# Kernel tuning notes

Measured on AMD Instinct MI355X. Metric: run time of the kernel, lower is better.

Reference implementation:

```python
import jax, jax.numpy as jnp
import numpy as np

N_NODES = 100000
N_EDGES = 500000
D = 128


def setup_inputs() -> dict:
    key = jax.random.key(0)
    ks = jax.random.split(key, 6)
    x = jax.random.normal(ks[0], (N_NODES, D), dtype=jnp.float32)
    edge_index = jax.random.randint(ks[1], (2, N_EDGES), 0, N_NODES, dtype=jnp.int64)
    edge_label = jax.random.randint(ks[2], (N_EDGES,), 0, 2, dtype=jnp.int64)
    # MLP params (dim_in -> dim_in, 2 layers, has_act=True, has_bias=True)
    scale = 1.0 / np.sqrt(D)
    W1 = jax.random.normal(ks[3], (D, D), dtype=jnp.float32) * scale
    b1 = jnp.zeros((D,), dtype=jnp.float32)
    W2 = jax.random.normal(ks[4], (D, D), dtype=jnp.float32) * scale
    b2 = jnp.zeros((D,), dtype=jnp.float32)
    return {"x": x, "edge_index": edge_index, "edge_label": edge_label,
            "W1": W1, "b1": b1, "W2": W2, "b2": b2}


def reference(x, edge_index, edge_label, W1, b1, W2, b2):
    # post-MP MLP on all node features (has_act=True -> ReLU after each layer)
    h = jax.nn.relu(x @ W1 + b1)          # [N, D]
    h = jax.nn.relu(h @ W2 + b2)          # [N, D]
    # gather endpoints: batch.x[edge_index] -> [2, E, D]
    v1 = h[edge_index[0]]                  # [E, D]
    v2 = h[edge_index[1]]                  # [E, D]
    # dot decode: sum(v1 * v2, dim=-1)
    pred = jnp.sum(v1 * v2, axis=-1)       # [E]
    return pred, edge_label
```

## Files before the change

### kernel.cpp

```cpp
#include <hip/hip_runtime.h>

typedef __attribute__((ext_vector_type(8))) short short8;
typedef __attribute__((ext_vector_type(4))) float floatx4;

#define D 128
#define NWAVES 4

__device__ unsigned short g_wq[2 * D * D];

__device__ __forceinline__ unsigned short f2bf(float f) {
  unsigned u = __float_as_uint(f);
  u += 0x7FFFu + ((u >> 16) & 1u);
  return (unsigned short)(u >> 16);
}

__global__ __launch_bounds__(256) void prep_w(const float* __restrict__ W1,
                                              const float* __restrict__ W2) {
  const int t = blockIdx.x * 256 + threadIdx.x;
  const int layer = t >> 14;
  const int r = t & 16383;
  const int fragid = r >> 9;
  const int lane = (r >> 3) & 63;
  const int e = r & 7;
  const int kk = fragid >> 3, n0 = fragid & 7;
  const int k = kk * 32 + (lane >> 4) * 8 + e;
  const int n = n0 * 16 + (lane & 15);
  const float* W = layer ? W2 : W1;
  g_wq[t] = f2bf(W[k * D + n]);
}

__device__ __forceinline__ short8 cvt_a(const floatx4& f0, const floatx4& f1) {
  short8 a;
  a[0] = (short)f2bf(f0[0]); a[1] = (short)f2bf(f0[1]);
  a[2] = (short)f2bf(f0[2]); a[3] = (short)f2bf(f0[3]);
  a[4] = (short)f2bf(f1[0]); a[5] = (short)f2bf(f1[1]);
  a[6] = (short)f2bf(f1[2]); a[7] = (short)f2bf(f1[3]);
  return a;
}

__global__ __launch_bounds__(256, 2) void mlp_fused(
    const float* __restrict__ x,
    const float* __restrict__ b1, const float* __restrict__ b2,
    unsigned short* __restrict__ h, int nNodes, int npairs) {
  __shared__ unsigned short sH[NWAVES][16 * D];
  const int tid = threadIdx.x;
  const int wave = tid >> 6, lane = tid & 63;
  const int quad = lane >> 4, l16 = lane & 15;

  const int p = blockIdx.x * NWAVES + wave;
  if (p >= npairs) return;

  const short8* wq1 = (const short8*)g_wq;
  const short8* wq2 = (const short8*)(g_wq + 16384);
  unsigned short* mysH = sH[wave];

  const int mbase = p * 32;
  const int m0 = mbase + l16;
  const int m1 = m0 + 16;
  short8 a0[4], a1[4];
  {
    const floatx4* xp0 = (const floatx4*)(x + (size_t)m0 * D + quad * 8);
    const floatx4* xp1 = (const floatx4*)(x + (size_t)m1 * D + quad * 8);
    const bool v0 = (m0 < nNodes), v1 = (m1 < nNodes);
    floatx4 xf0[8], xf1[8];
    #pragma unroll
    for (int i = 0; i < 8; ++i) {
      const int o = (i >> 1) * 8 + (i & 1);
      xf0[i] = v0 ? xp0[o] : (floatx4){0.f, 0.f, 0.f, 0.f};
      xf1[i] = v1 ? xp1[o] : (floatx4){0.f, 0.f, 0.f, 0.f};
    }
    #pragma unroll
    for (int kk = 0; kk < 4; ++kk) {
      a0[kk] = cvt_a(xf0[2 * kk], xf0[2 * kk + 1]);
      a1[kk] = cvt_a(xf1[2 * kk], xf1[2 * kk + 1]);
    }
  }
  short8 bf[32];
  #pragma unroll
  for (int i = 0; i < 32; ++i) bf[i] = wq1[i * 64 + lane];
  __builtin_amdgcn_sched_barrier(0);
  floatx4 acc0[8], acc1[8];
  #pragma unroll
  for (int n0 = 0; n0 < 8; ++n0) {
    acc0[n0] = (floatx4){0.f, 0.f, 0.f, 0.f};
    acc1[n0] = (floatx4){0.f, 0.f, 0.f, 0.f};
  }
  #pragma unroll
  for (int kk = 0; kk < 4; ++kk) {
    #pragma unroll
    for (int n0 = 0; n0 < 8; ++n0) {
      acc0[n0] = __builtin_amdgcn_mfma_f32_16x16x32_bf16(a0[kk], bf[kk * 8 + n0], acc0[n0], 0, 0, 0);
      acc1[n0] = __builtin_amdgcn_mfma_f32_16x16x32_bf16(a1[kk], bf[kk * 8 + n0], acc1[n0], 0, 0, 0);
    }
  }
  __builtin_amdgcn_sched_barrier(0);
  #pragma unroll
  for (int i = 0; i < 32; ++i) bf[i] = wq2[i * 64 + lane];
  __builtin_amdgcn_sched_barrier(0);
  float bias1[8];
  #pragma unroll
  for (int n0 = 0; n0 < 8; ++n0) bias1[n0] = b1[n0 * 16 + l16];
  short8 af0[4], af1[4];
  #pragma unroll
  for (int n0 = 0; n0 < 8; ++n0) {
    #pragma unroll
    for (int r = 0; r < 4; ++r) {
      float v = acc0[n0][r] + bias1[n0];
      v = v > 0.f ? v : 0.f;
      const int row = quad * 4 + r;
      const int g = 2 * n0 + (l16 >> 3);
      mysH[row * D + (((g ^ row) & 15) << 3) + (l16 & 7)] = f2bf(v);
    }
  }
  #pragma unroll
  for (int kk = 0; kk < 4; ++kk)
    af0[kk] = *(const short8*)&mysH[l16 * D + ((((kk * 4 + quad) ^ l16) & 15) << 3)];
  #pragma unroll
  for (int n0 = 0; n0 < 8; ++n0) {
    #pragma unroll
    for (int r = 0; r < 4; ++r) {
      float v = acc1[n0][r] + bias1[n0];
      v = v > 0.f ? v : 0.f;
      const int row = quad * 4 + r;
      const int g = 2 * n0 + (l16 >> 3);
      mysH[row * D + (((g ^ row) & 15) << 3) + (l16 & 7)] = f2bf(v);
    }
  }
  #pragma unroll
  for (int kk = 0; kk < 4; ++kk)
    af1[kk] = *(const short8*)&mysH[l16 * D + ((((kk * 4 + quad) ^ l16) & 15) << 3)];
  #pragma unroll
  for (int n0 = 0; n0 < 8; ++n0) {
    acc0[n0] = (floatx4){0.f, 0.f, 0.f, 0.f};
    acc1[n0] = (floatx4){0.f, 0.f, 0.f, 0.f};
  }
  #pragma unroll
  for (int kk = 0; kk < 4; ++kk) {
    #pragma unroll
    for (int n0 = 0; n0 < 8; ++n0) {
      acc0[n0] = __builtin_amdgcn_mfma_f32_16x16x32_bf16(af0[kk], bf[kk * 8 + n0], acc0[n0], 0, 0, 0);
      acc1[n0] = __builtin_amdgcn_mfma_f32_16x16x32_bf16(af1[kk], bf[kk * 8 + n0], acc1[n0], 0, 0, 0);
    }
  }
  __builtin_amdgcn_sched_barrier(0);
  float bias2[8];
  #pragma unroll
  for (int n0 = 0; n0 < 8; ++n0) bias2[n0] = b2[n0 * 16 + l16];
  #pragma unroll
  for (int n0 = 0; n0 < 8; ++n0) {
    #pragma unroll
    for (int r = 0; r < 4; ++r) {
      float v = acc0[n0][r] + bias2[n0];
      v = v > 0.f ? v : 0.f;
      const int row = quad * 4 + r;
      const int g = 2 * n0 + (l16 >> 3);
      mysH[row * D + (((g ^ row) & 15) << 3) + (l16 & 7)] = f2bf(v);
    }
  }
  #pragma unroll
  for (int i = 0; i < 4; ++i) {
    const int row = i * 4 + quad;
    short8 vrow = *(const short8*)&mysH[row * D + (((l16 ^ row) & 15) << 3)];
    const int g = mbase + row;
    if (g < nNodes) *(short8*)&h[(size_t)g * D + l16 * 8] = vrow;
  }
  #pragma unroll
  for (int n0 = 0; n0 < 8; ++n0) {
    #pragma unroll
    for (int r = 0; r < 4; ++r) {
      float v = acc1[n0][r] + bias2[n0];
      v = v > 0.f ? v : 0.f;
      const int row = quad * 4 + r;
      const int g = 2 * n0 + (l16 >> 3);
      mysH[row * D + (((g ^ row) & 15) << 3) + (l16 & 7)] = f2bf(v);
    }
  }
  #pragma unroll
  for (int i = 0; i < 4; ++i) {
    const int row = i * 4 + quad;
    short8 vrow = *(const short8*)&mysH[row * D + (((l16 ^ row) & 15) << 3)];
    const int g = mbase + 16 + row;
    if (g < nNodes) *(short8*)&h[(size_t)g * D + l16 * 8] = vrow;
  }
}

__device__ __forceinline__ float dot2bf(unsigned a, unsigned b, float acc) {
  float a0 = __uint_as_float(a << 16);
  float a1 = __uint_as_float(a & 0xFFFF0000u);
  float b0 = __uint_as_float(b << 16);
  float b1 = __uint_as_float(b & 0xFFFF0000u);
  acc = fmaf(a0, b0, acc);
  acc = fmaf(a1, b1, acc);
  return acc;
}

__device__ __forceinline__ float edge_dot(const uint4& a, const uint4& b) {
  float acc = 0.f;
  acc = dot2bf(a.x, b.x, acc);
  acc = dot2bf(a.y, b.y, acc);
  acc = dot2bf(a.z, b.z, acc);
  acc = dot2bf(a.w, b.w, acc);
  acc += __shfl_xor(acc, 8);
  acc += __shfl_xor(acc, 4);
  acc += __shfl_xor(acc, 2);
  acc += __shfl_xor(acc, 1);
  return acc;
}

__global__ __launch_bounds__(256) void edge_kernel(
    const unsigned short* __restrict__ h2, const int* __restrict__ eidx,
    const int* __restrict__ elabel, float* __restrict__ out, int E) {
  const int t = blockIdx.x * 256 + threadIdx.x;
  {
    const int E4 = E & ~3;
    for (int li = t * 4; li < E4; li += gridDim.x * 256 * 4) {
      int4 lv = *(const int4*)&elabel[li];
      float4 fv = make_float4((float)lv.x, (float)lv.y, (float)lv.z, (float)lv.w);
      *(float4*)&out[E + li] = fv;
    }
    if (t < (E & 3)) out[E + E4 + t] = (float)elabel[E4 + t];
  }
  const int sub = threadIdx.x & 15;
  const int grp = t >> 4;
  const int e0 = grp * 8;
  if (e0 + 8 <= E) {
    const int4 s0 = *(const int4*)&eidx[e0];
    const int4 s1 = *(const int4*)&eidx[e0 + 4];
    const int4 t0 = *(const int4*)&eidx[E + e0];
    const int4 t1 = *(const int4*)&eidx[E + e0 + 4];
    int s[8] = {s0.x, s0.y, s0.z, s0.w, s1.x, s1.y, s1.z, s1.w};
    int d[8] = {t0.x, t0.y, t0.z, t0.w, t1.x, t1.y, t1.z, t1.w};
    uint4 va[8], vb[8];
    #pragma unroll
    for (int i = 0; i < 8; ++i) {
      va[i] = *(const uint4*)(h2 + (((size_t)(unsigned)s[i]) << 7) + sub * 8);
      vb[i] = *(const uint4*)(h2 + (((size_t)(unsigned)d[i]) << 7) + sub * 8);
    }
    #pragma unroll
    for (int i = 0; i < 8; ++i) {
      float acc = edge_dot(va[i], vb[i]);
      if (sub == 0) out[e0 + i] = acc;
    }
  } else if (e0 < E) {
    for (int e = e0; e < E; ++e) {
      const int s = eidx[e];
      const int d = eidx[E + e];
      const uint4 ua = *(const uint4*)(h2 + (((size_t)(unsigned)s) << 7) + sub * 8);
      const uint4 ub = *(const uint4*)(h2 + (((size_t)(unsigned)d) << 7) + sub * 8);
      float acc = edge_dot(ua, ub);
      if (sub == 0) out[e] = acc;
    }
  }
}

extern "C" void kernel_launch(void* const* d_in, const int* in_sizes, int n_in,
                              void* d_out, int out_size, void* d_ws, size_t ws_size,
                              hipStream_t stream) {
  const float* x  = (const float*)d_in[0];
  const int* eidx = (const int*)d_in[1];
  const int* elab = (const int*)d_in[2];
  const float* W1 = (const float*)d_in[3];
  const float* b1 = (const float*)d_in[4];
  const float* W2 = (const float*)d_in[5];
  const float* b2 = (const float*)d_in[6];
  float* out = (float*)d_out;

  const int nNodes = in_sizes[0] / D;
  const int E = in_sizes[2];
  const int npairs = (nNodes + 31) / 32;

  unsigned short* h = (unsigned short*)d_ws;

  prep_w<<<128, 256, 0, stream>>>(W1, W2);

  const int nblk = (npairs + NWAVES - 1) / NWAVES;
  mlp_fused<<<nblk, 256, 0, stream>>>(x, b1, b2, h, nNodes, npairs);

  const int edgeBlocks = (E + 127) / 128;
  edge_kernel<<<edgeBlocks, 256, 0, stream>>>(h, eidx, elab, out, E);
}
```

Before: 152.6 us.

## Bucket-sort edges by source node and remap edge blocks across XCDs

Adds histogram, scan and scatter kernels that bucket edge ids by the upper bits of the source node index. The edge kernel then processes edges in that order, which is meant to improve L2 locality of source-row gathers. It also remaps block ids so that consecutive logical blocks are spread by a stride of eight, presumably so each XCD works on a contiguous range of buckets. The cost is three extra launches, global atomics, an extra indirection for edge ids and scattered output writes.

Measured after the change: 343.1 us. 2.25x slower.

```diff
diff --git a/kernel.cpp b/kernel.cpp
--- a/kernel.cpp
+++ b/kernel.cpp
@@ -5,8 +5,13 @@
 
 #define D 128
 #define NWAVES 4
+#define NB 512
+#define SORT_CAP 524288
 
 __device__ unsigned short g_wq[2 * D * D];
+__device__ int g_cnt[NB];
+__device__ int g_cur[NB];
+__device__ int g_sorted[SORT_CAP];
 
 __device__ __forceinline__ unsigned short f2bf(float f) {
   unsigned u = __float_as_uint(f);
@@ -16,6 +21,9 @@
 
 __global__ __launch_bounds__(256) void prep_w(const float* __restrict__ W1,
                                               const float* __restrict__ W2) {
+  if (blockIdx.x == 0) {
+    for (int i = threadIdx.x; i < NB; i += 256) g_cnt[i] = 0;
+  }
   const int t = blockIdx.x * 256 + threadIdx.x;
   const int layer = t >> 14;
   const int r = t & 16383;
@@ -29,6 +37,41 @@
   g_wq[t] = f2bf(W[k * D + n]);
 }
 
+__global__ __launch_bounds__(256) void e_hist(const int* __restrict__ eidx, int E) {
+  __shared__ int lc[NB];
+  for (int i = threadIdx.x; i < NB; i += 256) lc[i] = 0;
+  __syncthreads();
+  for (int e = blockIdx.x * 256 + threadIdx.x; e < E; e += gridDim.x * 256)
+    atomicAdd(&lc[(((unsigned)eidx[e]) >> 8) & (NB - 1)], 1);
+  __syncthreads();
+  for (int i = threadIdx.x; i < NB; i += 256)
+    if (lc[i]) atomicAdd(&g_cnt[i], lc[i]);
+}
+
+__global__ __launch_bounds__(NB) void e_scan() {
+  __shared__ int tmp[NB];
+  const int t = threadIdx.x;
+  const int v = g_cnt[t];
+  tmp[t] = v;
+  __syncthreads();
+  #pragma unroll
+  for (int off = 1; off < NB; off <<= 1) {
+    int add = (t >= off) ? tmp[t - off] : 0;
+    __syncthreads();
+    tmp[t] += add;
+    __syncthreads();
+  }
+  g_cur[t] = tmp[t] - v;
+}
+
+__global__ __launch_bounds__(256) void e_scatter(const int* __restrict__ eidx, int E) {
+  for (int e = blockIdx.x * 256 + threadIdx.x; e < E; e += gridDim.x * 256) {
+    const int b = (((unsigned)eidx[e]) >> 8) & (NB - 1);
+    const int pos = atomicAdd(&g_cur[b], 1);
+    g_sorted[pos] = e;
+  }
+}
+
 __device__ __forceinline__ short8 cvt_a(const floatx4& f0, const floatx4& f1) {
   short8 a;
   a[0] = (short)f2bf(f0[0]); a[1] = (short)f2bf(f0[1]);
@@ -209,8 +252,10 @@
 
 __global__ __launch_bounds__(256) void edge_kernel(
     const unsigned short* __restrict__ h2, const int* __restrict__ eidx,
-    const int* __restrict__ elabel, float* __restrict__ out, int E) {
-  const int t = blockIdx.x * 256 + threadIdx.x;
+    const int* __restrict__ elabel, float* __restrict__ out, int E,
+    int use_sorted) {
+  const int tid = threadIdx.x;
+  const int t = blockIdx.x * 256 + tid;
   {
     const int E4 = E & ~3;
     for (int li = t * 4; li < E4; li += gridDim.x * 256 * 4) {
@@ -220,16 +265,25 @@
     }
     if (t < (E & 3)) out[E + E4 + t] = (float)elabel[E4 + t];
   }
-  const int sub = threadIdx.x & 15;
-  const int grp = t >> 4;
+  const int q = gridDim.x >> 3;
+  const int lb = (blockIdx.x & 7) * q + (blockIdx.x >> 3);
+  const int sub = tid & 15;
+  const int grp = (lb * 256 + tid) >> 4;
   const int e0 = grp * 8;
   if (e0 + 8 <= E) {
-    const int4 s0 = *(const int4*)&eidx[e0];
-    const int4 s1 = *(const int4*)&eidx[e0 + 4];
-    const int4 t0 = *(const int4*)&eidx[E + e0];
-    const int4 t1 = *(const int4*)&eidx[E + e0 + 4];
-    int s[8] = {s0.x, s0.y, s0.z, s0.w, s1.x, s1.y, s1.z, s1.w};
-    int d[8] = {t0.x, t0.y, t0.z, t0.w, t1.x, t1.y, t1.z, t1.w};
+    int ei[8];
+    if (use_sorted) {
+      const int4 i0 = *(const int4*)&g_sorted[e0];
+      const int4 i1 = *(const int4*)&g_sorted[e0 + 4];
+      ei[0]=i0.x; ei[1]=i0.y; ei[2]=i0.z; ei[3]=i0.w;
+      ei[4]=i1.x; ei[5]=i1.y; ei[6]=i1.z; ei[7]=i1.w;
+    } else {
+      #pragma unroll
+      for (int i = 0; i < 8; ++i) ei[i] = e0 + i;
+    }
+    int s[8], d[8];
+    #pragma unroll
+    for (int i = 0; i < 8; ++i) { s[i] = eidx[ei[i]]; d[i] = eidx[E + ei[i]]; }
     uint4 va[8], vb[8];
     #pragma unroll
     for (int i = 0; i < 8; ++i) {
@@ -239,16 +293,17 @@
     #pragma unroll
     for (int i = 0; i < 8; ++i) {
       float acc = edge_dot(va[i], vb[i]);
-      if (sub == 0) out[e0 + i] = acc;
+      if (sub == 0) out[ei[i]] = acc;
     }
   } else if (e0 < E) {
     for (int e = e0; e < E; ++e) {
-      const int s = eidx[e];
-      const int d = eidx[E + e];
+      const int id = use_sorted ? g_sorted[e] : e;
+      const int s = eidx[id];
+      const int d = eidx[E + id];
       const uint4 ua = *(const uint4*)(h2 + (((size_t)(unsigned)s) << 7) + sub * 8);
       const uint4 ub = *(const uint4*)(h2 + (((size_t)(unsigned)d) << 7) + sub * 8);
       float acc = edge_dot(ua, ub);
-      if (sub == 0) out[e] = acc;
+      if (sub == 0) out[id] = acc;
     }
   }
 }
@@ -268,14 +323,22 @@
   const int nNodes = in_sizes[0] / D;
   const int E = in_sizes[2];
   const int npairs = (nNodes + 31) / 32;
+  const int use_sorted = (E <= SORT_CAP) ? 1 : 0;
 
   unsigned short* h = (unsigned short*)d_ws;
 
   prep_w<<<128, 256, 0, stream>>>(W1, W2);
+
+  if (use_sorted) {
+    e_hist<<<256, 256, 0, stream>>>(eidx, E);
+    e_scan<<<1, NB, 0, stream>>>();
+    e_scatter<<<256, 256, 0, stream>>>(eidx, E);
+  }
 
   const int nblk = (npairs + NWAVES - 1) / NWAVES;
   mlp_fused<<<nblk, 256, 0, stream>>>(x, b1, b2, h, nNodes, npairs);
 
-  const int edgeBlocks = (E + 127) / 128;
-  edge_kernel<<<edgeBlocks, 256, 0, stream>>>(h, eidx, elab, out, E);
-}
+  int eb = (E + 127) / 128;
+  eb = (eb + 7) & ~7;
+  edge_kernel<<<eb, 256, 0, stream>>>(h, eidx, elab, out, E, use_sorted);
+}
```

## Shrink MLP tile to 16 rows per wave and stream weights in halves

Applied to the files above, without the earlier changes.

Each wave in the fused MLP kernel now handles one 16-row tile instead of two, and the weight fragments are loaded in two 16-fragment halves instead of all 32 at once. Launch bounds are raised from 2 to 3 blocks per SIMD. This cuts register pressure to allow more resident waves for latency hiding. In exchange, every wave reloads the full weight matrices for half as many rows, doubling weight-fragment traffic, and each MFMA burst is shorter.

Result: faster. 149.5 us (-2.0%).

```diff
diff --git a/kernel.cpp b/kernel.cpp
--- a/kernel.cpp
+++ b/kernel.cpp
@@ -38,88 +38,113 @@
   return a;
 }
 
-__global__ __launch_bounds__(256, 2) void mlp_fused(
+__global__ __launch_bounds__(256, 3) void mlp_fused(
     const float* __restrict__ x,
     const float* __restrict__ b1, const float* __restrict__ b2,
-    unsigned short* __restrict__ h, int nNodes, int npairs) {
+    unsigned short* __restrict__ h, int nNodes, int ntiles) {
   __shared__ unsigned short sH[NWAVES][16 * D];
   const int tid = threadIdx.x;
   const int wave = tid >> 6, lane = tid & 63;
   const int quad = lane >> 4, l16 = lane & 15;
 
   const int p = blockIdx.x * NWAVES + wave;
-  if (p >= npairs) return;
+  if (p >= ntiles) return;
 
   const short8* wq1 = (const short8*)g_wq;
   const short8* wq2 = (const short8*)(g_wq + 16384);
   unsigned short* mysH = sH[wave];
 
-  const int mbase = p * 32;
+  const int mbase = p * 16;
   const int m0 = mbase + l16;
-  const int m1 = m0 + 16;
-  short8 a0[4], a1[4];
+  short8 a[4];
   {
-    const floatx4* xp0 = (const floatx4*)(x + (size_t)m0 * D + quad * 8);
-    const floatx4* xp1 = (const floatx4*)(x + (size_t)m1 * D + quad * 8);
-    const bool v0 = (m0 < nNodes), v1 = (m1 < nNodes);
-    floatx4 xf0[8], xf1[8];
+    const floatx4* xp = (const floatx4*)(x + (size_t)m0 * D + quad * 8);
+    const bool v = (m0 < nNodes);
+    floatx4 xf[8];
     #pragma unroll
     for (int i = 0; i < 8; ++i) {
       const int o = (i >> 1) * 8 + (i & 1);
-      xf0[i] = v0 ? xp0[o] : (floatx4){0.f, 0.f, 0.f, 0.f};
-      xf1[i] = v1 ? xp1[o] : (floatx4){0.f, 0.f, 0.f, 0.f};
-    }
-    #pragma unroll
-    for (int kk = 0; kk < 4; ++kk) {
-      a0[kk] = cvt_a(xf0[2 * kk], xf0[2 * kk + 1]);
-      a1[kk] = cvt_a(xf1[2 * kk], xf1[2 * kk + 1]);
-    }
-  }
-  short8 bf[32];
-  #pragma unroll
-  for (int i = 0; i < 32; ++i) bf[i] = wq1[i * 64 + lane];
-  __builtin_amdgcn_sched_barrier(0);
-  floatx4 acc0[8], acc1[8];
+      xf[i] = v ? xp[o] : (floatx4){0.f, 0.f, 0.f, 0.f};
+    }
+    #pragma unroll
+    for (int kk = 0; kk < 4; ++kk) a[kk] = cvt_a(xf[2 * kk], xf[2 * kk + 1]);
+  }
+  floatx4 acc[8];
+  #pragma unroll
+  for (int n0 = 0; n0 < 8; ++n0) acc[n0] = (floatx4){0.f, 0.f, 0.f, 0.f};
+  short8 bf[16];
+  #pragma unroll
+  for (int kk = 0; kk < 4; ++kk)
+    #pragma unroll
+    for (int j = 0; j < 4; ++j) bf[kk * 4 + j] = wq1[(kk * 8 + j) * 64 + lane];
+  __builtin_amdgcn_sched_barrier(0);
+  #pragma unroll
+  for (int kk = 0; kk < 4; ++kk)
+    #pragma unroll
+    for (int j = 0; j < 4; ++j)
+      acc[j] = __builtin_amdgcn_mfma_f32_16x16x32_bf16(a[kk], bf[kk * 4 + j], acc[j], 0, 0, 0);
+  __builtin_amdgcn_sched_barrier(0);
+  #pragma unroll
+  for (int kk = 0; kk < 4; ++kk)
+    #pragma unroll
+    for (int j = 0; j < 4; ++j) bf[kk * 4 + j] = wq1[(kk * 8 + 4 + j) * 64 + lane];
+  __builtin_amdgcn_sched_barrier(0);
+  #pragma unroll
+  for (int kk = 0; kk < 4; ++kk)
+    #pragma unroll
+    for (int j = 0; j < 4; ++j)
+      acc[4 + j] = __builtin_amdgcn_mfma_f32_16x16x32_bf16(a[kk], bf[kk * 4 + j], acc[4 + j], 0, 0, 0);
+  __builtin_amdgcn_sched_barrier(0);
+  float bias1[8];
+  #pragma unroll
+  for (int n0 = 0; n0 < 8; ++n0) bias1[n0] = b1[n0 * 16 + l16];
   #pragma unroll
   for (int n0 = 0; n0 < 8; ++n0) {
-    acc0[n0] = (floatx4){0.f, 0.f, 0.f, 0.f};
-    acc1[n0] = (floatx4){0.f, 0.f, 0.f, 0.f};
-  }
-  #pragma unroll
-  for (int kk = 0; kk < 4; ++kk) {
-    #pragma unroll
-    for (int n0 = 0; n0 < 8; ++n0) {
-      acc0[n0] = __builtin_amdgcn_mfma_f32_16x16x32_bf16(a0[kk], bf[kk * 8 + n0], acc0[n0], 0, 0, 0);
-      acc1[n0] = __builtin_amdgcn_mfma_f32_16x16x32_bf16(a1[kk], bf[kk * 8 + n0], acc1[n0], 0, 0, 0);
-    }
-  }
-  __builtin_amdgcn_sched_barrier(0);
-  #pragma unroll
-  for (int i = 0; i < 32; ++i) bf[i] = wq2[i * 64 + lane];
-  __builtin_amdgcn_sched_barrier(0);
-  float bias1[8];
-  #pragma unroll
-  for (int n0 = 0; n0 < 8; ++n0) bias1[n0] = b1[n0 * 16 + l16];
-  short8 af0[4], af1[4];
-  #pragma unroll
-  for (int n0 = 0; n0 < 8; ++n0) {
     #pragma unroll
     for (int r = 0; r < 4; ++r) {
-      float v = acc0[n0][r] + bias1[n0];
+      float v = acc[n0][r] + bias1[n0];
       v = v > 0.f ? v : 0.f;
       const int row = quad * 4 + r;
       const int g = 2 * n0 + (l16 >> 3);
       mysH[row * D + (((g ^ row) & 15) << 3) + (l16 & 7)] = f2bf(v);
     }
   }
-  #pragma unroll
-  for (int kk = 0; kk < 4; ++kk)
-    af0[kk] = *(const short8*)&mysH[l16 * D + ((((kk * 4 + quad) ^ l16) & 15) << 3)];
+  short8 af[4];
+  #pragma unroll
+  for (int kk = 0; kk < 4; ++kk)
+    af[kk] = *(const short8*)&mysH[l16 * D + ((((kk * 4 + quad) ^ l16) & 15) << 3)];
+  #pragma unroll
+  for (int n0 = 0; n0 < 8; ++n0) acc[n0] = (floatx4){0.f, 0.f, 0.f, 0.f};
+  #pragma unroll
+  for (int kk = 0; kk < 4; ++kk)
+    #pragma unroll
+    for (int j = 0; j < 4; ++j) bf[kk * 4 + j] = wq2[(kk * 8 + j) * 64 + lane];
+  __builtin_amdgcn_sched_barrier(0);
+  #pragma unroll
+  for (int kk = 0; kk < 4; ++kk)
+    #pragma unroll
+    for (int j = 0; j < 4; ++j)
+      acc[j] = __builtin_amdgcn_mfma_f32_16x16x32_bf16(af[kk], bf[kk * 4 + j], acc[j], 0, 0, 0);
+  __builtin_amdgcn_sched_barrier(0);
+  #pragma unroll
+  for (int kk = 0; kk < 4; ++kk)
+    #pragma unroll
+    for (int j = 0; j < 4; ++j) bf[kk * 4 + j] = wq2[(kk * 8 + 4 + j) * 64 + lane];
+  __builtin_amdgcn_sched_barrier(0);
+  #pragma unroll
+  for (int kk = 0; kk < 4; ++kk)
+    #pragma unroll
+    for (int j = 0; j < 4; ++j)
+      acc[4 + j] = __builtin_amdgcn_mfma_f32_16x16x32_bf16(af[kk], bf[kk * 4 + j], acc[4 + j], 0, 0, 0);
+  __builtin_amdgcn_sched_barrier(0);
+  float bias2[8];
+  #pragma unroll
+  for (int n0 = 0; n0 < 8; ++n0) bias2[n0] = b2[n0 * 16 + l16];
   #pragma unroll
   for (int n0 = 0; n0 < 8; ++n0) {
     #pragma unroll
     for (int r = 0; r < 4; ++r) {
-      float v = acc1[n0][r] + bias1[n0];
+      float v = acc[n0][r] + bias2[n0];
       v = v > 0.f ? v : 0.f;
       const int row = quad * 4 + r;
       const int g = 2 * n0 + (l16 >> 3);
@@ -127,59 +152,10 @@
     }
   }
   #pragma unroll
-  for (int kk = 0; kk < 4; ++kk)
-    af1[kk] = *(const short8*)&mysH[l16 * D + ((((kk * 4 + quad) ^ l16) & 15) << 3)];
-  #pragma unroll
-  for (int n0 = 0; n0 < 8; ++n0) {
-    acc0[n0] = (floatx4){0.f, 0.f, 0.f, 0.f};
-    acc1[n0] = (floatx4){0.f, 0.f, 0.f, 0.f};
-  }
-  #pragma unroll
-  for (int kk = 0; kk < 4; ++kk) {
-    #pragma unroll
-    for (int n0 = 0; n0 < 8; ++n0) {
-      acc0[n0] = __builtin_amdgcn_mfma_f32_16x16x32_bf16(af0[kk], bf[kk * 8 + n0], acc0[n0], 0, 0, 0);
-      acc1[n0] = __builtin_amdgcn_mfma_f32_16x16x32_bf16(af1[kk], bf[kk * 8 + n0], acc1[n0], 0, 0, 0);
-    }
-  }
-  __builtin_amdgcn_sched_barrier(0);
-  float bias2[8];
-  #pragma unroll
-  for (int n0 = 0; n0 < 8; ++n0) bias2[n0] = b2[n0 * 16 + l16];
-  #pragma unroll
-  for (int n0 = 0; n0 < 8; ++n0) {
-    #pragma unroll
-    for (int r = 0; r < 4; ++r) {
-      float v = acc0[n0][r] + bias2[n0];
-      v = v > 0.f ? v : 0.f;
-      const int row = quad * 4 + r;
-      const int g = 2 * n0 + (l16 >> 3);
-      mysH[row * D + (((g ^ row) & 15) << 3) + (l16 & 7)] = f2bf(v);
-    }
-  }
-  #pragma unroll
   for (int i = 0; i < 4; ++i) {
     const int row = i * 4 + quad;
     short8 vrow = *(const short8*)&mysH[row * D + (((l16 ^ row) & 15) << 3)];
     const int g = mbase + row;
-    if (g < nNodes) *(short8*)&h[(size_t)g * D + l16 * 8] = vrow;
-  }
-  #pragma unroll
-  for (int n0 = 0; n0 < 8; ++n0) {
-    #pragma unroll
-    for (int r = 0; r < 4; ++r) {
-      float v = acc1[n0][r] + bias2[n0];
-      v = v > 0.f ? v : 0.f;
-      const int row = quad * 4 + r;
-      const int g = 2 * n0 + (l16 >> 3);
-      mysH[row * D + (((g ^ row) & 15) << 3) + (l16 & 7)] = f2bf(v);
-    }
-  }
-  #pragma unroll
-  for (int i = 0; i < 4; ++i) {
-    const int row = i * 4 + quad;
-    short8 vrow = *(const short8*)&mysH[row * D + (((l16 ^ row) & 15) << 3)];
-    const int g = mbase + 16 + row;
     if (g < nNodes) *(short8*)&h[(size_t)g * D + l16 * 8] = vrow;
   }
 }
@@ -267,14 +243,14 @@
 
   const int nNodes = in_sizes[0] / D;
   const int E = in_sizes[2];
-  const int npairs = (nNodes + 31) / 32;
+  const int ntiles = (nNodes + 15) / 16;
 
   unsigned short* h = (unsigned short*)d_ws;
 
   prep_w<<<128, 256, 0, stream>>>(W1, W2);
 
-  const int nblk = (npairs + NWAVES - 1) / NWAVES;
-  mlp_fused<<<nblk, 256, 0, stream>>>(x, b1, b2, h, nNodes, npairs);
+  const int nblk = (ntiles + NWAVES - 1) / NWAVES;
+  mlp_fused<<<nblk, 256, 0, stream>>>(x, b1, b2, h, nNodes, ntiles);
 
   const int edgeBlocks = (E + 127) / 128;
   edge_kernel<<<edgeBlocks, 256, 0, stream>>>(h, eidx, elab, out, E);
```
